# Optimization experiments

Hardware: AMD Instinct MI355X
Metric: run time of the kernel (lower is better)

## Reference

```python
import jax, jax.numpy as jnp
import numpy as np

D_MODEL = 1024
NUM_HEADS = 16
LN_EPS = 1e-5


def setup_inputs() -> dict:
    key = jax.random.key(0)
    ks = jax.random.split(key, 7)
    B, S, D = 8, 1024, D_MODEL
    x = jax.random.normal(ks[0], (B, S, D), dtype=jnp.float32)
    # LayerNorm params (torch defaults: weight=1, bias=0; randomize slightly)
    ln_gamma = jnp.ones((D,), jnp.float32) + 0.02 * jax.random.normal(ks[1], (D,), jnp.float32)
    ln_beta = 0.02 * jax.random.normal(ks[2], (D,), jnp.float32)
    # nn.MultiheadAttention params: packed in_proj [3D, D], out_proj [D, D]
    scale = 1.0 / np.sqrt(D)
    in_proj_w = scale * jax.random.normal(ks[3], (3 * D, D), dtype=jnp.float32)
    in_proj_b = jnp.zeros((3 * D,), jnp.float32)
    out_proj_w = scale * jax.random.normal(ks[4], (D, D), dtype=jnp.float32)
    out_proj_b = jnp.zeros((D,), jnp.float32)
    return {
        "x": x,
        "ln_gamma": ln_gamma,
        "ln_beta": ln_beta,
        "in_proj_w": in_proj_w,
        "in_proj_b": in_proj_b,
        "out_proj_w": out_proj_w,
        "out_proj_b": out_proj_b,
    }


def reference(x, ln_gamma, ln_beta, in_proj_w, in_proj_b, out_proj_w, out_proj_b):
    B, S, D = x.shape
    H = NUM_HEADS
    Dh = D // H

    residual = x
    # LayerNorm (torch eps=1e-5)
    mu = jnp.mean(x, axis=-1, keepdims=True)
    var = jnp.mean(jnp.square(x - mu), axis=-1, keepdims=True)
    xn = (x - mu) * jax.lax.rsqrt(var + LN_EPS) * ln_gamma + ln_beta

    # Packed QKV projection: y = xn @ in_proj_w.T + in_proj_b
    qkv = jnp.einsum("bsd,ed->bse", xn, in_proj_w) + in_proj_b  # [B,S,3D]
    q, k, v = jnp.split(qkv, 3, axis=-1)

    def heads(t):  # [B,S,D] -> [B,H,S,Dh]
        return t.reshape(B, S, H, Dh).transpose(0, 2, 1, 3)

    q, k, v = heads(q), heads(k), heads(v)

    scores = jnp.einsum("bhsd,bhtd->bhst", q, k) / np.sqrt(Dh)  # [B,H,S,S]
    probs = jax.nn.softmax(scores, axis=-1)
    ctx = jnp.einsum("bhst,bhtd->bhsd", probs, v)  # [B,H,S,Dh]
    ctx = ctx.transpose(0, 2, 1, 3).reshape(B, S, D)

    attn_out = jnp.einsum("bsd,ed->bse", ctx, out_proj_w) + out_proj_b
    # (need_weights=True would also expose probs.mean over heads; math above
    #  matches the explicit non-flash path torch falls back to)
    return attn_out + residual
```

## Files before the change

### kernel.cpp

```cpp
#include <hip/hip_runtime.h>
#include <hip/hip_bf16.h>

typedef __bf16 bf16;
typedef __bf16 bf16x8 __attribute__((ext_vector_type(8)));
typedef __bf16 bf16x4 __attribute__((ext_vector_type(4)));
typedef float  f32x4  __attribute__((ext_vector_type(4)));

#define D_MODEL 1024
#define S_LEN   1024
#define NHEAD   16
#define DH      64

#define AS1 __attribute__((address_space(1)))
#define AS3 __attribute__((address_space(3)))

__global__ void cvt_kernel(const float* __restrict__ w1, bf16* __restrict__ o1, int n1,
                           const float* __restrict__ w2, bf16* __restrict__ o2, int n2) {
    int i = blockIdx.x * blockDim.x + threadIdx.x;
    const int stride = gridDim.x * blockDim.x;
    for (; i < n1 + n2; i += stride) {
        const float4 v = (i < n1) ? ((const float4*)w1)[i] : ((const float4*)w2)[i - n1];
        bf16x4 r;
        r[0] = (bf16)v.x; r[1] = (bf16)v.y; r[2] = (bf16)v.z; r[3] = (bf16)v.w;
        if (i < n1) ((bf16x4*)o1)[i] = r; else ((bf16x4*)o2)[i - n1] = r;
    }
}

__global__ __launch_bounds__(256) void ln_kernel(const float* __restrict__ x,
        const float* __restrict__ gamma, const float* __restrict__ beta,
        bf16* __restrict__ xn) {
    const int row = blockIdx.x;
    const int tid = threadIdx.x;
    const float4 v = ((const float4*)(x + (size_t)row * D_MODEL))[tid];
    float s  = v.x + v.y + v.z + v.w;
    float s2 = v.x*v.x + v.y*v.y + v.z*v.z + v.w*v.w;
    #pragma unroll
    for (int d = 1; d < 64; d <<= 1) { s += __shfl_xor(s, d); s2 += __shfl_xor(s2, d); }
    __shared__ float red[8];
    const int wave = tid >> 6;
    if ((tid & 63) == 0) { red[wave] = s; red[4 + wave] = s2; }
    __syncthreads();
    s  = red[0] + red[1] + red[2] + red[3];
    s2 = red[4] + red[5] + red[6] + red[7];
    const float mu   = s * (1.0f / D_MODEL);
    const float var  = s2 * (1.0f / D_MODEL) - mu * mu;
    const float rstd = rsqrtf(var + 1e-5f);
    const float4 g = ((const float4*)gamma)[tid];
    const float4 b = ((const float4*)beta)[tid];
    bf16x4 o;
    o[0] = (bf16)((v.x - mu) * rstd * g.x + b.x);
    o[1] = (bf16)((v.y - mu) * rstd * g.y + b.y);
    o[2] = (bf16)((v.z - mu) * rstd * g.z + b.z);
    o[3] = (bf16)((v.w - mu) * rstd * g.w + b.w);
    ((bf16x4*)(xn + (size_t)row * D_MODEL))[tid] = o;
}

#define GEMM_MAIN_LOOP(Ab, Wb, K)                                                        \
    f32x4 acc[4][4] = {};                                                                \
    for (int kt = 0; kt < (K); kt += 64) {                                               \
        _Pragma("unroll")                                                                \
        for (int i = 0; i < 4; ++i) {                                                    \
            const int L = i * 256 + tid;                                                 \
            const int r = L >> 3, blk = L & 7;                                           \
            const int src = (blk ^ (r & 7)) * 8;                                         \
            __builtin_amdgcn_global_load_lds(                                            \
                (const AS1 void*)((Ab) + (size_t)r * (K) + kt + src),                    \
                (AS3 void*)(As + L * 8), 16, 0, 0);                                      \
            __builtin_amdgcn_global_load_lds(                                            \
                (const AS1 void*)((Wb) + (size_t)r * (K) + kt + src),                    \
                (AS3 void*)(Bs + L * 8), 16, 0, 0);                                      \
        }                                                                                \
        __syncthreads();                                                                 \
        _Pragma("unroll")                                                                \
        for (int kk = 0; kk < 2; ++kk) {                                                 \
            bf16x8 af[4], bfm[4];                                                        \
            _Pragma("unroll")                                                            \
            for (int m = 0; m < 4; ++m) {                                                \
                const int R = wr * 64 + m * 16 + (lane & 15);                            \
                af[m] = *(const bf16x8*)(As + R * 64 +                                   \
                            (((kk * 4 + (lane >> 4)) ^ (R & 7)) << 3));                  \
            }                                                                            \
            _Pragma("unroll")                                                            \
            for (int n = 0; n < 4; ++n) {                                                \
                const int R = wc * 64 + n * 16 + (lane & 15);                            \
                bfm[n] = *(const bf16x8*)(Bs + R * 64 +                                  \
                            (((kk * 4 + (lane >> 4)) ^ (R & 7)) << 3));                  \
            }                                                                            \
            _Pragma("unroll")                                                            \
            for (int m = 0; m < 4; ++m)                                                  \
                _Pragma("unroll")                                                        \
                for (int n = 0; n < 4; ++n)                                              \
                    acc[m][n] = __builtin_amdgcn_mfma_f32_16x16x32_bf16(                 \
                        af[m], bfm[n], acc[m][n], 0, 0, 0);                              \
        }                                                                                \
        __syncthreads();                                                                 \
    }

#define XCD_REMAP()                                                                      \
    const int f = blockIdx.y * gridDim.x + blockIdx.x;                                   \
    const int xcd = f & 7;                                                               \
    const int rank = f >> 3;                                                             \
    const int brow = (xcd * 8 + (rank & 7)) * 128;                                       \
    const int bcol = (rank >> 3) * 128;

__global__ __launch_bounds__(512, 2) void gemm_qkv(
        const bf16* __restrict__ A, const bf16* __restrict__ W,
        const float* __restrict__ bias,
        bf16* __restrict__ q, bf16* __restrict__ k, bf16* __restrict__ vt) {
    __shared__ bf16 smem[65536];
    bf16* As = smem;
    bf16* Bs = smem + 32768;
    const int tid = threadIdx.x;
    const int lane = tid & 63;
    const int wid = tid >> 6;
    const int wm = wid >> 2, wn = wid & 3;
    const int c = lane & 15, h = lane >> 4;
    const int f = blockIdx.x;
    const int xcd = f & 7, loc = f >> 3;
    const int mt = xcd * 4 + (loc & 3);
    const int nt = loc >> 2;
    const int brow = mt * 256, bcol = nt * 256;
    const bf16* Ab = A + (size_t)brow * 1024;
    const bf16* Wb = W + (size_t)bcol * 1024;

#define LOADT(XS, XG, LI, BUF, KTE) do {                                                 \
    const int row_ = (LI) * 64 + (tid >> 3);                                             \
    __builtin_amdgcn_global_load_lds(                                                    \
        (const AS1 void*)((XG) + (size_t)row_ * 1024 + (KTE) +                           \
                          (((tid & 7) ^ (row_ & 7)) << 3)),                              \
        (AS3 void*)((XS) + (BUF) * 16384 + (LI) * 4096 + tid * 8), 16, 0, 0);            \
} while (0)

#define LDA4(BUF, MH, AF) do {                                                           \
    _Pragma("unroll")                                                                    \
    for (int m_ = 0; m_ < 4; ++m_) {                                                     \
        const int R_ = wm * 128 + (MH) * 64 + m_ * 16 + c;                               \
        _Pragma("unroll")                                                                \
        for (int k_ = 0; k_ < 2; ++k_)                                                   \
            AF[m_][k_] = *(const bf16x8*)(As + (BUF) * 16384 + R_ * 64 +                 \
                           (((k_ * 4 + h) ^ (R_ & 7)) << 3));                            \
    }                                                                                    \
} while (0)

#define LDB2(BUF, NH, BF) do {                                                           \
    _Pragma("unroll")                                                                    \
    for (int n_ = 0; n_ < 2; ++n_) {                                                     \
        const int R_ = wn * 64 + (NH) * 32 + n_ * 16 + c;                                \
        _Pragma("unroll")                                                                \
        for (int k_ = 0; k_ < 2; ++k_)                                                   \
            BF[n_][k_] = *(const bf16x8*)(Bs + (BUF) * 16384 + R_ * 64 +                 \
                           (((k_ * 4 + h) ^ (R_ & 7)) << 3));                            \
    }                                                                                    \
} while (0)

#define MFMAQ(MH, NH, AF, BF) do {                                                       \
    __builtin_amdgcn_s_setprio(1);                                                       \
    _Pragma("unroll")                                                                    \
    for (int m_ = 0; m_ < 4; ++m_)                                                       \
        _Pragma("unroll")                                                                \
        for (int n_ = 0; n_ < 2; ++n_)                                                   \
            _Pragma("unroll")                                                            \
            for (int k_ = 0; k_ < 2; ++k_)                                               \
                acc[(MH)*4 + m_][(NH)*2 + n_] =                                          \
                    __builtin_amdgcn_mfma_f32_16x16x32_bf16(                             \
                        AF[m_][k_], BF[n_][k_],                                          \
                        acc[(MH)*4 + m_][(NH)*2 + n_], 0, 0, 0);                         \
    __builtin_amdgcn_s_setprio(0);                                                       \
} while (0)

#define SB0() __builtin_amdgcn_sched_barrier(0)
#define BAR() __builtin_amdgcn_s_barrier()
#define LGKM0() do { asm volatile("s_waitcnt lgkmcnt(0)" ::: "memory"); SB0(); } while (0)

    f32x4 acc[8][4] = {};
    #pragma unroll
    for (int li = 0; li < 4; ++li) { LOADT(As, Ab, li, 0, 0); LOADT(Bs, Wb, li, 0, 0); }

    for (int t = 0; t < 16; ++t) {
        const int cur = t & 1, nxt = cur ^ 1;
        const int kte = (t + 1) * 64;
        bf16x8 af0[4][2], af1[4][2], bf0[2][2], bf1[2][2];
        if (t < 15) {
            LOADT(As, Ab, 0, nxt, kte); LOADT(As, Ab, 1, nxt, kte);
            asm volatile("s_waitcnt vmcnt(2)" ::: "memory");
        } else {
            asm volatile("s_waitcnt vmcnt(0)" ::: "memory");
        }
        BAR();
        LDA4(cur, 0, af0); LDB2(cur, 0, bf0);
        SB0();
        if (t < 15) { LOADT(Bs, Wb, 0, nxt, kte); LOADT(Bs, Wb, 1, nxt, kte); }
        BAR();
        LGKM0();
        MFMAQ(0, 0, af0, bf0);
        BAR();
        LDB2(cur, 1, bf1);
        SB0();
        if (t < 15) { LOADT(As, Ab, 2, nxt, kte); LOADT(As, Ab, 3, nxt, kte); }
        BAR();
        LGKM0();
        MFMAQ(0, 1, af0, bf1);
        BAR();
        LDA4(cur, 1, af1);
        SB0();
        if (t < 15) { LOADT(Bs, Wb, 2, nxt, kte); LOADT(Bs, Wb, 3, nxt, kte); }
        BAR();
        LGKM0();
        MFMAQ(1, 1, af1, bf1);
        BAR();
        MFMAQ(1, 0, af1, bf0);
    }
#undef LOADT
#undef LDA4
#undef LDB2
#undef MFMAQ
#undef SB0
#undef BAR
#undef LGKM0

    __syncthreads();
    if (nt >= 8) {
        #pragma unroll
        for (int m = 0; m < 8; ++m) {
            const int rowg = brow + wm * 128 + m * 16 + h * 4;
            const int b = rowg >> 10, s0 = rowg & 1023;
            #pragma unroll
            for (int n = 0; n < 4; ++n) {
                const int colg = bcol + wn * 64 + n * 16 + c;
                const float bb = bias[colg];
                const int e = colg & 1023;
                const int bh = b * NHEAD + (e >> 6), dh = e & 63;
                bf16x4 pk;
                #pragma unroll
                for (int j = 0; j < 4; ++j) pk[j] = (bf16)(acc[m][n][j] + bb);
                *(bf16x4*)(vt + ((size_t)bh * DH + dh) * S_LEN + s0) = pk;
            }
        }
    } else {
        const float qsc = (nt < 4) ? 0.1803368801111244f : 1.0f;
        bf16* dst = (nt < 4) ? q : k;
        bf16* pat = smem + wid * 8192;
        #pragma unroll
        for (int m = 0; m < 8; ++m)
            #pragma unroll
            for (int n = 0; n < 4; ++n) {
                const int col = n * 16 + c;
                const float bb = bias[bcol + wn * 64 + col];
                #pragma unroll
                for (int j = 0; j < 4; ++j) {
                    const int rl = m * 16 + h * 4 + j;
                    pat[rl * 64 + ((((col >> 3) ^ (rl & 7)) << 3) | (col & 7))] =
                        (bf16)((acc[m][n][j] + bb) * qsc);
                }
            }
        const int hh8 = ((bcol + wn * 64) & 1023) >> 6;
        #pragma unroll
        for (int i = 0; i < 16; ++i) {
            const int row = i * 8 + (lane >> 3);
            const int blk = lane & 7;
            const bf16x8 vv = *(const bf16x8*)(pat + row * 64 + ((blk ^ (row & 7)) << 3));
            const int rowg = brow + wm * 128 + row;
            const int b = rowg >> 10, s = rowg & 1023;
            *(bf16x8*)(dst + ((size_t)(b * NHEAD + hh8) * S_LEN + s) * DH + blk * 8) = vv;
        }
    }
}

__global__ __launch_bounds__(256, 4) void gemm_out(
        const bf16* __restrict__ A, const bf16* __restrict__ W,
        const float* __restrict__ bias, const float* __restrict__ resid,
        float* __restrict__ out) {
    __shared__ bf16 smem[2 * 128 * 64];
    bf16* As = smem;
    bf16* Bs = smem + 128 * 64;
    const int tid = threadIdx.x;
    const int lane = tid & 63;
    const int wave = tid >> 6;
    const int wr = wave >> 1, wc = wave & 1;
    XCD_REMAP()
    const bf16* Ab = A + (size_t)brow * 1024;
    const bf16* Wb = W + (size_t)bcol * 1024;

    GEMM_MAIN_LOOP(Ab, Wb, 1024)

    #pragma unroll
    for (int m = 0; m < 4; ++m) {
        #pragma unroll
        for (int n = 0; n < 4; ++n) {
            const int col = bcol + wc * 64 + n * 16 + (lane & 15);
            const float bb = bias[col];
            #pragma unroll
            for (int j = 0; j < 4; ++j) {
                const int row = brow + wr * 64 + m * 16 + (lane >> 4) * 4 + j;
                const size_t idx = (size_t)row * D_MODEL + col;
                out[idx] = acc[m][n][j] + bb + resid[idx];
            }
        }
    }
}

__global__ __launch_bounds__(256, 3) void attn_kernel(
        const bf16* __restrict__ Q, const bf16* __restrict__ Kv,
        const bf16* __restrict__ Vt, bf16* __restrict__ ctx) {
    __shared__ bf16 KsB[2][64 * 64];
    __shared__ bf16 VsB[2][64 * 64];
    __shared__ bf16 PtB[4][32 * 64];
    const int tid = threadIdx.x;
    const int lane = tid & 63;
    const int w = tid >> 6;
    const int c = lane & 15;
    const int h = lane >> 4;
    const int bh = blockIdx.x;
    const int bb = bh >> 4, hd = bh & 15;
    const int q0 = blockIdx.y * 128 + w * 32;

    const bf16* Qh = Q + ((size_t)bh * S_LEN + q0) * DH;
    const char* Kb = (const char*)(Kv + (size_t)bh * S_LEN * DH);
    const char* Vb = (const char*)(Vt + (size_t)bh * DH * S_LEN);
    char* pw = (char*)&PtB[w][0];

    bf16x8 qf[2][2];
    #pragma unroll
    for (int nq = 0; nq < 2; ++nq)
        #pragma unroll
        for (int kk = 0; kk < 2; ++kk)
            qf[nq][kk] = *(const bf16x8*)(Qh + (16 * nq + c) * DH + kk * 32 + h * 8);

    bf16x8 ones;
    #pragma unroll
    for (int j = 0; j < 8; ++j) ones[j] = (bf16)1.0f;

    f32x4 O[2][4] = {};
    f32x4 lacc[2] = {};

#define STAGE(BB, KT) do {                                                               \
    _Pragma("unroll")                                                                    \
    for (int i = 0; i < 2; ++i) {                                                        \
        const int row = w * 16 + i * 8 + (lane >> 3);                                    \
        const int sw = ((lane & 7) ^ (row & 7)) << 4;                                    \
        const int lo = w * 2048 + i * 1024 + lane * 16;                                  \
        __builtin_amdgcn_global_load_lds(                                                \
            (const AS1 void*)(Kb + (size_t)((KT) + row) * 128 + sw),                     \
            (AS3 void*)((char*)&KsB[BB][0] + lo), 16, 0, 0);                             \
        __builtin_amdgcn_global_load_lds(                                                \
            (const AS1 void*)(Vb + (size_t)row * 2048 + (KT) * 2 + sw),                  \
            (AS3 void*)((char*)&VsB[BB][0] + lo), 16, 0, 0);                             \
    } } while (0)

    STAGE(0, 0);
    for (int t = 0; t < 16; ++t) {
        if (t < 15) {
            STAGE((t + 1) & 1, (t + 1) * 64);
            asm volatile("s_waitcnt vmcnt(4)" ::: "memory");
        } else {
            asm volatile("s_waitcnt vmcnt(0)" ::: "memory");
        }
        __builtin_amdgcn_s_barrier();
        const char* Ksb = (const char*)&KsB[t & 1][0];
        const char* Vsb = (const char*)&VsB[t & 1][0];

        f32x4 sf[2][4] = {};
        __builtin_amdgcn_s_setprio(1);
        #pragma unroll
        for (int kk = 0; kk < 2; ++kk) {
            bf16x8 kf[4];
            #pragma unroll
            for (int a = 0; a < 4; ++a)
                kf[a] = *(const bf16x8*)(Ksb + (16 * a + c) * 128 +
                                         (((4 * kk + h) ^ (c & 7)) << 4));
            #pragma unroll
            for (int nq = 0; nq < 2; ++nq)
                #pragma unroll
                for (int a = 0; a < 4; ++a)
                    sf[nq][a] = __builtin_amdgcn_mfma_f32_16x16x32_bf16(
                        kf[a], qf[nq][kk], sf[nq][a], 0, 0, 0);
        }
        __builtin_amdgcn_s_setprio(0);

        #pragma unroll
        for (int nq = 0; nq < 2; ++nq) {
            #pragma unroll
            for (int a = 0; a < 4; ++a) {
                bf16x4 pk;
                #pragma unroll
                for (int r = 0; r < 4; ++r)
                    pk[r] = (bf16)__builtin_amdgcn_exp2f(sf[nq][a][r]);
                *(bf16x4*)(pw + (16 * nq + c) * 128 +
                           (((2 * a + (h >> 1)) ^ (c & 7)) << 4) + 8 * (h & 1)) = pk;
            }
        }

        __builtin_amdgcn_s_setprio(1);
        #pragma unroll
        for (int kk = 0; kk < 2; ++kk) {
            bf16x8 pf[2], vf[4];
            #pragma unroll
            for (int mq = 0; mq < 2; ++mq)
                pf[mq] = *(const bf16x8*)(pw + (16 * mq + c) * 128 +
                                          (((4 * kk + h) ^ (c & 7)) << 4));
            #pragma unroll
            for (int f2 = 0; f2 < 4; ++f2)
                vf[f2] = *(const bf16x8*)(Vsb + (16 * f2 + c) * 128 +
                                          (((4 * kk + h) ^ (c & 7)) << 4));
            #pragma unroll
            for (int mq = 0; mq < 2; ++mq) {
                #pragma unroll
                for (int f2 = 0; f2 < 4; ++f2)
                    O[mq][f2] = __builtin_amdgcn_mfma_f32_16x16x32_bf16(
                        pf[mq], vf[f2], O[mq][f2], 0, 0, 0);
                lacc[mq] = __builtin_amdgcn_mfma_f32_16x16x32_bf16(
                    pf[mq], ones, lacc[mq], 0, 0, 0);
            }
        }
        __builtin_amdgcn_s_setprio(0);
        asm volatile("s_waitcnt lgkmcnt(0)" ::: "memory");
        __builtin_amdgcn_s_barrier();
    }
#undef STAGE

    #pragma unroll
    for (int mq = 0; mq < 2; ++mq) {
        float iv[4];
        #pragma unroll
        for (int r = 0; r < 4; ++r) iv[r] = 1.0f / lacc[mq][r];
        #pragma unroll
        for (int f2 = 0; f2 < 4; ++f2)
            #pragma unroll
            for (int r = 0; r < 4; ++r) {
                const int s = q0 + 16 * mq + 4 * h + r;
                ctx[((size_t)(bb * S_LEN + s)) * D_MODEL + hd * DH + 16 * f2 + c] =
                    (bf16)(O[mq][f2][r] * iv[r]);
            }
    }
}

extern "C" void kernel_launch(void* const* d_in, const int* in_sizes, int n_in,
                              void* d_out, int out_size, void* d_ws, size_t ws_size,
                              hipStream_t stream) {
    const float* x     = (const float*)d_in[0];
    const float* gamma = (const float*)d_in[1];
    const float* beta  = (const float*)d_in[2];
    const float* in_w  = (const float*)d_in[3];
    const float* in_b  = (const float*)d_in[4];
    const float* out_w = (const float*)d_in[5];
    const float* out_b = (const float*)d_in[6];
    float* out = (float*)d_out;

    char* ws = (char*)d_ws;
    bf16* wq  = (bf16*)(ws);
    bf16* wo  = (bf16*)(ws + 6291456);
    bf16* xn  = (bf16*)(ws + 8388608);
    bf16* q   = (bf16*)(ws + 25165824);
    bf16* kk  = (bf16*)(ws + 41943040);
    bf16* vt  = (bf16*)(ws + 58720256);
    bf16* ctx = xn;

    hipLaunchKernelGGL(cvt_kernel, dim3(512), dim3(256), 0, stream,
                       in_w, wq, 3072 * 1024 / 4, out_w, wo, 1024 * 1024 / 4);
    hipLaunchKernelGGL(ln_kernel, dim3(8192), dim3(256), 0, stream, x, gamma, beta, xn);
    hipLaunchKernelGGL(gemm_qkv, dim3(384), dim3(512), 0, stream, xn, wq, in_b, q, kk, vt);
    hipLaunchKernelGGL(attn_kernel, dim3(128, 8), dim3(256), 0, stream, q, kk, vt, ctx);
    hipLaunchKernelGGL(gemm_out, dim3(64, 8), dim3(256), 0, stream, ctx, wo, out_b, x, out);
}
```

Measured before the change: 157.9 us.

## Fuse LayerNorm with weight conversion, reorder QKV GEMM prefetch, widen attention blocks

Merges the weight fp32-to-bf16 conversion and LayerNorm into one launch, with extra blocks handling conversion, which removes a kernel launch and lets the two run concurrently. The QKV GEMM now issues all A-tile prefetches at the top of the iteration and all B-tile prefetches after the first LDS read, instead of interleaving them across the phases. The attention kernel goes from 4 to 8 waves per block, so each block covers 256 queries and the K/V staging of each tile is shared by twice as many waves. This halves the number of K/V tile loads per query, at the cost of more LDS per block and larger blocks that may lower occupancy.

```diff
diff --git a/kernel.cpp b/kernel.cpp
--- a/kernel.cpp
+++ b/kernel.cpp
@@ -14,45 +14,46 @@
 #define AS1 __attribute__((address_space(1)))
 #define AS3 __attribute__((address_space(3)))
 
-__global__ void cvt_kernel(const float* __restrict__ w1, bf16* __restrict__ o1, int n1,
-                           const float* __restrict__ w2, bf16* __restrict__ o2, int n2) {
-    int i = blockIdx.x * blockDim.x + threadIdx.x;
-    const int stride = gridDim.x * blockDim.x;
-    for (; i < n1 + n2; i += stride) {
-        const float4 v = (i < n1) ? ((const float4*)w1)[i] : ((const float4*)w2)[i - n1];
-        bf16x4 r;
-        r[0] = (bf16)v.x; r[1] = (bf16)v.y; r[2] = (bf16)v.z; r[3] = (bf16)v.w;
-        if (i < n1) ((bf16x4*)o1)[i] = r; else ((bf16x4*)o2)[i - n1] = r;
-    }
-}
-
-__global__ __launch_bounds__(256) void ln_kernel(const float* __restrict__ x,
-        const float* __restrict__ gamma, const float* __restrict__ beta,
-        bf16* __restrict__ xn) {
-    const int row = blockIdx.x;
+__global__ __launch_bounds__(256) void ln_cvt_kernel(
+        const float* __restrict__ x, const float* __restrict__ gamma,
+        const float* __restrict__ beta, bf16* __restrict__ xn,
+        const float* __restrict__ w1, bf16* __restrict__ o1, int n1,
+        const float* __restrict__ w2, bf16* __restrict__ o2, int n2) {
     const int tid = threadIdx.x;
-    const float4 v = ((const float4*)(x + (size_t)row * D_MODEL))[tid];
-    float s  = v.x + v.y + v.z + v.w;
-    float s2 = v.x*v.x + v.y*v.y + v.z*v.z + v.w*v.w;
-    #pragma unroll
-    for (int d = 1; d < 64; d <<= 1) { s += __shfl_xor(s, d); s2 += __shfl_xor(s2, d); }
-    __shared__ float red[8];
-    const int wave = tid >> 6;
-    if ((tid & 63) == 0) { red[wave] = s; red[4 + wave] = s2; }
-    __syncthreads();
-    s  = red[0] + red[1] + red[2] + red[3];
-    s2 = red[4] + red[5] + red[6] + red[7];
-    const float mu   = s * (1.0f / D_MODEL);
-    const float var  = s2 * (1.0f / D_MODEL) - mu * mu;
-    const float rstd = rsqrtf(var + 1e-5f);
-    const float4 g = ((const float4*)gamma)[tid];
-    const float4 b = ((const float4*)beta)[tid];
-    bf16x4 o;
-    o[0] = (bf16)((v.x - mu) * rstd * g.x + b.x);
-    o[1] = (bf16)((v.y - mu) * rstd * g.y + b.y);
-    o[2] = (bf16)((v.z - mu) * rstd * g.z + b.z);
-    o[3] = (bf16)((v.w - mu) * rstd * g.w + b.w);
-    ((bf16x4*)(xn + (size_t)row * D_MODEL))[tid] = o;
+    if (blockIdx.x < 8192) {
+        const int row = blockIdx.x;
+        const float4 v = ((const float4*)(x + (size_t)row * D_MODEL))[tid];
+        float s  = v.x + v.y + v.z + v.w;
+        float s2 = v.x*v.x + v.y*v.y + v.z*v.z + v.w*v.w;
+        #pragma unroll
+        for (int d = 1; d < 64; d <<= 1) { s += __shfl_xor(s, d); s2 += __shfl_xor(s2, d); }
+        __shared__ float red[8];
+        const int wave = tid >> 6;
+        if ((tid & 63) == 0) { red[wave] = s; red[4 + wave] = s2; }
+        __syncthreads();
+        s  = red[0] + red[1] + red[2] + red[3];
+        s2 = red[4] + red[5] + red[6] + red[7];
+        const float mu   = s * (1.0f / D_MODEL);
+        const float var  = s2 * (1.0f / D_MODEL) - mu * mu;
+        const float rstd = rsqrtf(var + 1e-5f);
+        const float4 g = ((const float4*)gamma)[tid];
+        const float4 b = ((const float4*)beta)[tid];
+        bf16x4 o;
+        o[0] = (bf16)((v.x - mu) * rstd * g.x + b.x);
+        o[1] = (bf16)((v.y - mu) * rstd * g.y + b.y);
+        o[2] = (bf16)((v.z - mu) * rstd * g.z + b.z);
+        o[3] = (bf16)((v.w - mu) * rstd * g.w + b.w);
+        ((bf16x4*)(xn + (size_t)row * D_MODEL))[tid] = o;
+    } else {
+        int i = (blockIdx.x - 8192) * 256 + tid;
+        const int stride = 1024 * 256;
+        for (; i < n1 + n2; i += stride) {
+            const float4 v = (i < n1) ? ((const float4*)w1)[i] : ((const float4*)w2)[i - n1];
+            bf16x4 r;
+            r[0] = (bf16)v.x; r[1] = (bf16)v.y; r[2] = (bf16)v.z; r[3] = (bf16)v.w;
+            if (i < n1) ((bf16x4*)o1)[i] = r; else ((bf16x4*)o2)[i - n1] = r;
+        }
+    }
 }
 
 #define GEMM_MAIN_LOOP(Ab, Wb, K)                                                        \
@@ -174,7 +175,9 @@
 
     f32x4 acc[8][4] = {};
     #pragma unroll
-    for (int li = 0; li < 4; ++li) { LOADT(As, Ab, li, 0, 0); LOADT(Bs, Wb, li, 0, 0); }
+    for (int li = 0; li < 4; ++li) LOADT(As, Ab, li, 0, 0);
+    #pragma unroll
+    for (int li = 0; li < 4; ++li) LOADT(Bs, Wb, li, 0, 0);
 
     for (int t = 0; t < 16; ++t) {
         const int cur = t & 1, nxt = cur ^ 1;
@@ -182,28 +185,30 @@
         bf16x8 af0[4][2], af1[4][2], bf0[2][2], bf1[2][2];
         if (t < 15) {
             LOADT(As, Ab, 0, nxt, kte); LOADT(As, Ab, 1, nxt, kte);
-            asm volatile("s_waitcnt vmcnt(2)" ::: "memory");
+            LOADT(As, Ab, 2, nxt, kte); LOADT(As, Ab, 3, nxt, kte);
+            asm volatile("s_waitcnt vmcnt(4)" ::: "memory");
         } else {
             asm volatile("s_waitcnt vmcnt(0)" ::: "memory");
         }
         BAR();
         LDA4(cur, 0, af0); LDB2(cur, 0, bf0);
         SB0();
-        if (t < 15) { LOADT(Bs, Wb, 0, nxt, kte); LOADT(Bs, Wb, 1, nxt, kte); }
+        if (t < 15) {
+            LOADT(Bs, Wb, 0, nxt, kte); LOADT(Bs, Wb, 1, nxt, kte);
+            LOADT(Bs, Wb, 2, nxt, kte); LOADT(Bs, Wb, 3, nxt, kte);
+        }
         BAR();
         LGKM0();
         MFMAQ(0, 0, af0, bf0);
         BAR();
         LDB2(cur, 1, bf1);
         SB0();
-        if (t < 15) { LOADT(As, Ab, 2, nxt, kte); LOADT(As, Ab, 3, nxt, kte); }
         BAR();
         LGKM0();
         MFMAQ(0, 1, af0, bf1);
         BAR();
         LDA4(cur, 1, af1);
         SB0();
-        if (t < 15) { LOADT(Bs, Wb, 2, nxt, kte); LOADT(Bs, Wb, 3, nxt, kte); }
         BAR();
         LGKM0();
         MFMAQ(1, 1, af1, bf1);
@@ -299,12 +304,12 @@
     }
 }
 
-__global__ __launch_bounds__(256, 3) void attn_kernel(
+__global__ __launch_bounds__(512, 4) void attn_kernel(
         const bf16* __restrict__ Q, const bf16* __restrict__ Kv,
         const bf16* __restrict__ Vt, bf16* __restrict__ ctx) {
     __shared__ bf16 KsB[2][64 * 64];
     __shared__ bf16 VsB[2][64 * 64];
-    __shared__ bf16 PtB[4][32 * 64];
+    __shared__ bf16 PtB[8][32 * 64];
     const int tid = threadIdx.x;
     const int lane = tid & 63;
     const int w = tid >> 6;
@@ -312,7 +317,7 @@
     const int h = lane >> 4;
     const int bh = blockIdx.x;
     const int bb = bh >> 4, hd = bh & 15;
-    const int q0 = blockIdx.y * 128 + w * 32;
+    const int q0 = blockIdx.y * 256 + w * 32;
 
     const bf16* Qh = Q + ((size_t)bh * S_LEN + q0) * DH;
     const char* Kb = (const char*)(Kv + (size_t)bh * S_LEN * DH);
@@ -334,24 +339,21 @@
     f32x4 lacc[2] = {};
 
 #define STAGE(BB, KT) do {                                                               \
-    _Pragma("unroll")                                                                    \
-    for (int i = 0; i < 2; ++i) {                                                        \
-        const int row = w * 16 + i * 8 + (lane >> 3);                                    \
-        const int sw = ((lane & 7) ^ (row & 7)) << 4;                                    \
-        const int lo = w * 2048 + i * 1024 + lane * 16;                                  \
-        __builtin_amdgcn_global_load_lds(                                                \
-            (const AS1 void*)(Kb + (size_t)((KT) + row) * 128 + sw),                     \
-            (AS3 void*)((char*)&KsB[BB][0] + lo), 16, 0, 0);                             \
-        __builtin_amdgcn_global_load_lds(                                                \
-            (const AS1 void*)(Vb + (size_t)row * 2048 + (KT) * 2 + sw),                  \
-            (AS3 void*)((char*)&VsB[BB][0] + lo), 16, 0, 0);                             \
-    } } while (0)
+    const int row = tid >> 3;                                                            \
+    const int sw = ((tid & 7) ^ (row & 7)) << 4;                                         \
+    __builtin_amdgcn_global_load_lds(                                                    \
+        (const AS1 void*)(Kb + (size_t)((KT) + row) * 128 + sw),                         \
+        (AS3 void*)((char*)&KsB[BB][0] + tid * 16), 16, 0, 0);                           \
+    __builtin_amdgcn_global_load_lds(                                                    \
+        (const AS1 void*)(Vb + (size_t)row * 2048 + (KT) * 2 + sw),                      \
+        (AS3 void*)((char*)&VsB[BB][0] + tid * 16), 16, 0, 0);                           \
+} while (0)
 
     STAGE(0, 0);
     for (int t = 0; t < 16; ++t) {
         if (t < 15) {
             STAGE((t + 1) & 1, (t + 1) * 64);
-            asm volatile("s_waitcnt vmcnt(4)" ::: "memory");
+            asm volatile("s_waitcnt vmcnt(2)" ::: "memory");
         } else {
             asm volatile("s_waitcnt vmcnt(0)" ::: "memory");
         }
@@ -455,10 +457,10 @@
     bf16* vt  = (bf16*)(ws + 58720256);
     bf16* ctx = xn;
 
-    hipLaunchKernelGGL(cvt_kernel, dim3(512), dim3(256), 0, stream,
+    hipLaunchKernelGGL(ln_cvt_kernel, dim3(9216), dim3(256), 0, stream,
+                       x, gamma, beta, xn,
                        in_w, wq, 3072 * 1024 / 4, out_w, wo, 1024 * 1024 / 4);
-    hipLaunchKernelGGL(ln_kernel, dim3(8192), dim3(256), 0, stream, x, gamma, beta, xn);
     hipLaunchKernelGGL(gemm_qkv, dim3(384), dim3(512), 0, stream, xn, wq, in_b, q, kk, vt);
-    hipLaunchKernelGGL(attn_kernel, dim3(128, 8), dim3(256), 0, stream, q, kk, vt, ctx);
+    hipLaunchKernelGGL(attn_kernel, dim3(128, 4), dim3(512), 0, stream, q, kk, vt, ctx);
     hipLaunchKernelGGL(gemm_out, dim3(64, 8), dim3(256), 0, stream, ctx, wo, out_b, x, out);
 }
```

New measurement: 149.2 us. -5.5%, faster.
